# Optimization experiments

Measured on AMD Instinct MI355X. Metric: run time of the kernel, lower is better.

## Reference

```python
import jax, jax.numpy as jnp
import numpy as np

PI_2 = 3.14159 / 2  # matches the torch module's pi_2 constant
EPS = 1e-8          # F.cosine_similarity default eps


def setup_inputs() -> dict:
    key = jax.random.key(0)
    k1, k2 = jax.random.split(key)
    B, N, C, H, W = 32, 2000, 512, 7, 7
    key_t = jax.random.normal(k1, (B, C, H, W), dtype=jnp.float32)
    memory = jax.random.normal(k2, (N, C, H, W), dtype=jnp.float32)
    return {"key": key_t, "memory": memory}


def reference(key, memory):
    # Memory.read(key): cosine-similarity addressing + tan warp + softmax, then weighted read.
    B = key.shape[0]
    N = memory.shape[0]
    k = key.reshape(B, -1)        # [B, D], D = C*H*W
    m = memory.reshape(N, -1)     # [N, D]
    # cosine similarity with torch's eps clamping on norms
    dots = jnp.einsum('bd,nd->bn', k, m)                                   # [B, N]
    k_norm = jnp.maximum(jnp.sqrt(jnp.sum(k * k, axis=-1, keepdims=True)), EPS)  # [B, 1]
    m_norm = jnp.maximum(jnp.sqrt(jnp.sum(m * m, axis=-1)), EPS)                 # [N]
    cos = dots / (k_norm * m_norm[None, :])                                 # [B, N]
    w = jax.nn.softmax(jnp.tan(cos * PI_2), axis=1)                         # [B, N]
    # weighted read: sum_n w[b,n] * memory[n,c,h,w] -> [B, C, H, W]
    out = jnp.einsum('bn,nchw->bchw', w, memory)
    return out
```

## Files before the change

kernel.cpp:

```cpp
#include <hip/hip_runtime.h>
#include <math.h>

#define D_ELEMS 25088
#define D4      6272
#define N_MEM   2000
#define B_KEYS  32
#define PI_2F   1.570795f
#define EPSF    1e-8f
#define NSLICE  8
#define KSLICE  3136
#define KSTEPS  98

using short8 = __attribute__((ext_vector_type(8))) short;
using short4v = __attribute__((ext_vector_type(4))) short;
using f32x4  = __attribute__((ext_vector_type(4))) float;


__device__ inline short f2bf(float x) {
    union { float f; unsigned u; } v; v.f = x;
    unsigned r = v.u + 0x7fffu + ((v.u >> 16) & 1u);
    return (short)(r >> 16);
}

__global__ __launch_bounds__(256) void k_prep(const float* __restrict__ key,
                                              short* __restrict__ keyb) {
    const int i = blockIdx.x * 256 + threadIdx.x;
    const float4 f = ((const float4*)key)[i];
    short4v s; s[0] = f2bf(f.x); s[1] = f2bf(f.y); s[2] = f2bf(f.z); s[3] = f2bf(f.w);
    ((short4v*)keyb)[i] = s;
}

__global__ __launch_bounds__(64) void k_dots_mfma(const short* __restrict__ keyb,
                                                  const float* __restrict__ mem,
                                                  float* __restrict__ dots_part,
                                                  float* __restrict__ mn2_part) {
    const int nt   = blockIdx.x / NSLICE;
    const int s    = blockIdx.x % NSLICE;
    const int n0   = nt * 16;
    const int lane = threadIdx.x;
    const int quad = lane >> 4;
    const int l16  = lane & 15;
    const int k0   = s * KSLICE + quad * 8;

    const short* a0p = keyb + (size_t)l16 * D_ELEMS + k0;
    const short* a1p = keyb + (size_t)(16 + l16) * D_ELEMS + k0;
    const float4* bp = (const float4*)(mem + (size_t)(n0 + l16) * D_ELEMS + k0);

    f32x4 acc0 = {0.f, 0.f, 0.f, 0.f};
    f32x4 acc1 = {0.f, 0.f, 0.f, 0.f};
    float msq = 0.f;

    short8 a0 = *(const short8*)a0p;
    short8 a1 = *(const short8*)a1p;
    float4 f0 = bp[0], f1 = bp[1];

    for (int t = 0; t < KSTEPS; ++t) {
        const short8 a0c = a0, a1c = a1;
        const float4 f0c = f0, f1c = f1;
        if (t + 1 < KSTEPS) {
            const int ko = (t + 1) * 8;
            a0 = *(const short8*)(a0p + (t + 1) * 32);
            a1 = *(const short8*)(a1p + (t + 1) * 32);
            f0 = bp[ko]; f1 = bp[ko + 1];
        }
        msq += f0c.x * f0c.x + f0c.y * f0c.y + f0c.z * f0c.z + f0c.w * f0c.w
             + f1c.x * f1c.x + f1c.y * f1c.y + f1c.z * f1c.z + f1c.w * f1c.w;
        short8 b;
        b[0] = f2bf(f0c.x); b[1] = f2bf(f0c.y); b[2] = f2bf(f0c.z); b[3] = f2bf(f0c.w);
        b[4] = f2bf(f1c.x); b[5] = f2bf(f1c.y); b[6] = f2bf(f1c.z); b[7] = f2bf(f1c.w);
        acc0 = __builtin_amdgcn_mfma_f32_16x16x32_bf16(a0c, b, acc0, 0, 0, 0);
        acc1 = __builtin_amdgcn_mfma_f32_16x16x32_bf16(a1c, b, acc1, 0, 0, 0);
    }

    float* dp = dots_part + (size_t)(s * N_MEM + n0 + l16) * B_KEYS;
#pragma unroll
    for (int r = 0; r < 4; ++r) {
        dp[quad * 4 + r]      = acc0[r];
        dp[16 + quad * 4 + r] = acc1[r];
    }

    msq += __shfl_xor(msq, 16, 64);
    msq += __shfl_xor(msq, 32, 64);
    if (lane < 16) mn2_part[s * N_MEM + n0 + lane] = msq;
}

__global__ __launch_bounds__(512) void k_softmax(const float* __restrict__ key,
                                                 const float* __restrict__ dots_part,
                                                 const float* __restrict__ mn2_part,
                                                 float* __restrict__ w) {
    const int b   = blockIdx.x;
    const int tid = threadIdx.x;
    __shared__ float sred[512];
    __shared__ float xbuf[N_MEM];

    const float4* K4 = (const float4*)(key + (size_t)b * D_ELEMS);
    float ks = 0.f;
    for (int i = tid; i < D4; i += 512) {
        float4 kf = K4[i];
        ks += kf.x * kf.x + kf.y * kf.y + kf.z * kf.z + kf.w * kf.w;
    }
    sred[tid] = ks;
    __syncthreads();
    for (int o = 256; o; o >>= 1) {
        if (tid < o) sred[tid] += sred[tid + o];
        __syncthreads();
    }
    const float knorm = fmaxf(sqrtf(sred[0]), EPSF);
    __syncthreads();

    float mx = -1e30f;
    for (int n = tid; n < N_MEM; n += 512) {
        float ds = 0.f, ms = 0.f;
#pragma unroll
        for (int s = 0; s < NSLICE; ++s) ds += dots_part[(size_t)(s * N_MEM + n) * B_KEYS + b];
#pragma unroll
        for (int s = 0; s < NSLICE; ++s) ms += mn2_part[s * N_MEM + n];
        float mn = fmaxf(sqrtf(ms), EPSF);
        float x  = __tanf((ds / (knorm * mn)) * PI_2F);
        xbuf[n] = x;
        mx = fmaxf(mx, x);
    }
    sred[tid] = mx;
    __syncthreads();
    for (int o = 256; o; o >>= 1) {
        if (tid < o) sred[tid] = fmaxf(sred[tid], sred[tid + o]);
        __syncthreads();
    }
    mx = sred[0];
    __syncthreads();

    float sm = 0.f;
    for (int n = tid; n < N_MEM; n += 512) sm += __expf(xbuf[n] - mx);
    sred[tid] = sm;
    __syncthreads();
    for (int o = 256; o; o >>= 1) {
        if (tid < o) sred[tid] += sred[tid + o];
        __syncthreads();
    }
    const float inv = 1.f / sred[0];
    __syncthreads();

    for (int n = tid; n < N_MEM; n += 512)
        w[n * B_KEYS + b] = __expf(xbuf[n] - mx) * inv;
}

__global__ __launch_bounds__(256) void k_read(const float* __restrict__ mem,
                                              const float* __restrict__ w,
                                              float* __restrict__ partial,
                                              int nPerS) {
    const int db   = blockIdx.x % 98;
    const int s    = blockIdx.x / 98;
    const int n0   = s * nPerS;
    const int bg   = threadIdx.x >> 6;
    const int lane = threadIdx.x & 63;
    const int d4   = db * 64 + lane;

    const float4* M4 = (const float4*)mem;
    const float4* W4 = (const float4*)w;
    __shared__ float4 wls4[250 * 8];

    float acc[8][4];
#pragma unroll
    for (int i = 0; i < 8; ++i)
#pragma unroll
        for (int j = 0; j < 4; ++j) acc[i][j] = 0.f;

    for (int c0 = 0; c0 < nPerS; c0 += 250) {
        const int cn = min(250, nPerS - c0);
        __syncthreads();
        for (int i = threadIdx.x; i < cn * 8; i += 256)
            wls4[i] = W4[(n0 + c0) * 8 + i];
        __syncthreads();

        float4 mv = M4[(size_t)(n0 + c0) * D4 + d4];
        float4 wa = wls4[bg * 2];
        float4 wb = wls4[bg * 2 + 1];
        for (int nn = 0; nn < cn; ++nn) {
            const float4 mc = mv, wac = wa, wbc = wb;
            const int nx = (nn + 1 < cn) ? nn + 1 : nn;
            mv = M4[(size_t)(n0 + c0 + nx) * D4 + d4];
            wa = wls4[nx * 8 + bg * 2];
            wb = wls4[nx * 8 + bg * 2 + 1];
            const float wv[8] = {wac.x, wac.y, wac.z, wac.w,
                                 wbc.x, wbc.y, wbc.z, wbc.w};
#pragma unroll
            for (int i = 0; i < 8; ++i) {
                acc[i][0] += wv[i] * mc.x;
                acc[i][1] += wv[i] * mc.y;
                acc[i][2] += wv[i] * mc.z;
                acc[i][3] += wv[i] * mc.w;
            }
        }
    }

    float4* P4 = (float4*)partial;
#pragma unroll
    for (int i = 0; i < 8; ++i)
        P4[(size_t)(s * B_KEYS + bg * 8 + i) * D4 + d4] =
            make_float4(acc[i][0], acc[i][1], acc[i][2], acc[i][3]);
}

__global__ __launch_bounds__(256) void k_finish(const float* __restrict__ partial,
                                                float* __restrict__ out, int ns) {
    const int i = blockIdx.x * 256 + threadIdx.x;
    const float4* P4 = (const float4*)partial;
    float4 sum = P4[i];
    for (int s = 1; s < ns; ++s) {
        const float4 p = P4[(size_t)s * (B_KEYS * D4) + i];
        sum.x += p.x; sum.y += p.y; sum.z += p.z; sum.w += p.w;
    }
    ((float4*)out)[i] = sum;
}

extern "C" void kernel_launch(void* const* d_in, const int* in_sizes, int n_in,
                              void* d_out, int out_size, void* d_ws, size_t ws_size,
                              hipStream_t stream) {
    (void)in_sizes; (void)n_in; (void)out_size;
    const float* key = (const float*)d_in[0];
    const float* mem = (const float*)d_in[1];
    float* out = (float*)d_out;
    float* ws  = (float*)d_ws;

    short* keyb      = (short*)ws;
    float* dots_part = ws + 401408;
    float* mn2_part  = ws + 913408;
    float* w         = ws + 929408;
    float* part      = ws + 993408;

    int ns = 8;
    while (ns > 1 && (size_t)(993408 + (size_t)ns * 802816) * 4 > ws_size) ns >>= 1;
    const int nPerS = N_MEM / ns;

    k_prep     <<<784, 256, 0, stream>>>(key, keyb);
    k_dots_mfma<<<125 * NSLICE, 64, 0, stream>>>(keyb, mem, dots_part, mn2_part);
    k_softmax  <<<B_KEYS, 512, 0, stream>>>(key, dots_part, mn2_part, w);
    k_read     <<<98 * ns, 256, 0, stream>>>(mem, w, part, nPerS);
    k_finish   <<<784, 256, 0, stream>>>(part, out, ns);
}
```

Measured before the change: 420.3 us.

## Double K-split in dots kernel, add parallel reduce, unroll read loop by two

The MFMA dot kernel now splits the reduction dimension into 16 slices instead of 8, so it launches more blocks on the memory-bound first pass. A new k_reduce kernel sums the partial dots and norms across all threads, replacing the per-thread strided reduction inside the 32-block softmax kernel. The weighted-read kernel unrolls its loop by two with two memory prefetches in flight, fixes the chunk size at 250, and adds an occupancy hint of 3 blocks per SM. The cost is twice the partial-buffer traffic and one extra kernel launch.

```diff
diff --git a/kernel.cpp b/kernel.cpp
--- a/kernel.cpp
+++ b/kernel.cpp
@@ -7,9 +7,9 @@
 #define B_KEYS  32
 #define PI_2F   1.570795f
 #define EPSF    1e-8f
-#define NSLICE  8
-#define KSLICE  3136
-#define KSTEPS  98
+#define NSLICE  16
+#define KSLICE  1568
+#define KSTEPS  49
 
 using short8 = __attribute__((ext_vector_type(8))) short;
 using short4v = __attribute__((ext_vector_type(4))) short;
@@ -58,10 +58,10 @@
         const short8 a0c = a0, a1c = a1;
         const float4 f0c = f0, f1c = f1;
         if (t + 1 < KSTEPS) {
-            const int ko = (t + 1) * 8;
             a0 = *(const short8*)(a0p + (t + 1) * 32);
             a1 = *(const short8*)(a1p + (t + 1) * 32);
-            f0 = bp[ko]; f1 = bp[ko + 1];
+            f0 = bp[(t + 1) * 8];
+            f1 = bp[(t + 1) * 8 + 1];
         }
         msq += f0c.x * f0c.x + f0c.y * f0c.y + f0c.z * f0c.z + f0c.w * f0c.w
              + f1c.x * f1c.x + f1c.y * f1c.y + f1c.z * f1c.z + f1c.w * f1c.w;
@@ -84,9 +84,26 @@
     if (lane < 16) mn2_part[s * N_MEM + n0 + lane] = msq;
 }
 
+__global__ __launch_bounds__(256) void k_reduce(const float* __restrict__ dots_part,
+                                                const float* __restrict__ mn2_part,
+                                                float* __restrict__ dots,
+                                                float* __restrict__ mn2) {
+    const int gid = blockIdx.x * 256 + threadIdx.x;
+    float ds = 0.f;
+#pragma unroll
+    for (int s = 0; s < NSLICE; ++s) ds += dots_part[s * (N_MEM * B_KEYS) + gid];
+    dots[gid] = ds;
+    if (gid < N_MEM) {
+        float ms = 0.f;
+#pragma unroll
+        for (int s = 0; s < NSLICE; ++s) ms += mn2_part[s * N_MEM + gid];
+        mn2[gid] = ms;
+    }
+}
+
 __global__ __launch_bounds__(512) void k_softmax(const float* __restrict__ key,
-                                                 const float* __restrict__ dots_part,
-                                                 const float* __restrict__ mn2_part,
+                                                 const float* __restrict__ dots,
+                                                 const float* __restrict__ mn2,
                                                  float* __restrict__ w) {
     const int b   = blockIdx.x;
     const int tid = threadIdx.x;
@@ -110,13 +127,8 @@
 
     float mx = -1e30f;
     for (int n = tid; n < N_MEM; n += 512) {
-        float ds = 0.f, ms = 0.f;
-#pragma unroll
-        for (int s = 0; s < NSLICE; ++s) ds += dots_part[(size_t)(s * N_MEM + n) * B_KEYS + b];
-#pragma unroll
-        for (int s = 0; s < NSLICE; ++s) ms += mn2_part[s * N_MEM + n];
-        float mn = fmaxf(sqrtf(ms), EPSF);
-        float x  = __tanf((ds / (knorm * mn)) * PI_2F);
+        float mn = fmaxf(sqrtf(mn2[n]), EPSF);
+        float x  = __tanf((dots[n * B_KEYS + b] / (knorm * mn)) * PI_2F);
         xbuf[n] = x;
         mx = fmaxf(mx, x);
     }
@@ -144,10 +156,10 @@
         w[n * B_KEYS + b] = __expf(xbuf[n] - mx) * inv;
 }
 
-__global__ __launch_bounds__(256) void k_read(const float* __restrict__ mem,
-                                              const float* __restrict__ w,
-                                              float* __restrict__ partial,
-                                              int nPerS) {
+__global__ __launch_bounds__(256, 3) void k_read(const float* __restrict__ mem,
+                                                 const float* __restrict__ w,
+                                                 float* __restrict__ partial,
+                                                 int nPerS) {
     const int db   = blockIdx.x % 98;
     const int s    = blockIdx.x / 98;
     const int n0   = s * nPerS;
@@ -166,29 +178,45 @@
         for (int j = 0; j < 4; ++j) acc[i][j] = 0.f;
 
     for (int c0 = 0; c0 < nPerS; c0 += 250) {
-        const int cn = min(250, nPerS - c0);
+        const int cn = 250;
         __syncthreads();
         for (int i = threadIdx.x; i < cn * 8; i += 256)
             wls4[i] = W4[(n0 + c0) * 8 + i];
         __syncthreads();
 
-        float4 mv = M4[(size_t)(n0 + c0) * D4 + d4];
-        float4 wa = wls4[bg * 2];
-        float4 wb = wls4[bg * 2 + 1];
-        for (int nn = 0; nn < cn; ++nn) {
-            const float4 mc = mv, wac = wa, wbc = wb;
-            const int nx = (nn + 1 < cn) ? nn + 1 : nn;
-            mv = M4[(size_t)(n0 + c0 + nx) * D4 + d4];
-            wa = wls4[nx * 8 + bg * 2];
-            wb = wls4[nx * 8 + bg * 2 + 1];
-            const float wv[8] = {wac.x, wac.y, wac.z, wac.w,
-                                 wbc.x, wbc.y, wbc.z, wbc.w};
-#pragma unroll
-            for (int i = 0; i < 8; ++i) {
-                acc[i][0] += wv[i] * mc.x;
-                acc[i][1] += wv[i] * mc.y;
-                acc[i][2] += wv[i] * mc.z;
-                acc[i][3] += wv[i] * mc.w;
+        const float4* mp = M4 + (size_t)(n0 + c0) * D4 + d4;
+        float4 mv0 = mp[0];
+        float4 mv1 = mp[(size_t)D4];
+        for (int nn = 0; nn < cn; nn += 2) {
+            const float4 mc0 = mv0;
+            const int i2 = (nn + 2 < cn) ? nn + 2 : cn - 2;
+            mv0 = mp[(size_t)i2 * D4];
+            {
+                const float4 wa = wls4[nn * 8 + bg * 2];
+                const float4 wb = wls4[nn * 8 + bg * 2 + 1];
+                const float wv[8] = {wa.x, wa.y, wa.z, wa.w, wb.x, wb.y, wb.z, wb.w};
+#pragma unroll
+                for (int i = 0; i < 8; ++i) {
+                    acc[i][0] += wv[i] * mc0.x;
+                    acc[i][1] += wv[i] * mc0.y;
+                    acc[i][2] += wv[i] * mc0.z;
+                    acc[i][3] += wv[i] * mc0.w;
+                }
+            }
+            const float4 mc1 = mv1;
+            const int i3 = (nn + 3 < cn) ? nn + 3 : cn - 1;
+            mv1 = mp[(size_t)i3 * D4];
+            {
+                const float4 wa = wls4[(nn + 1) * 8 + bg * 2];
+                const float4 wb = wls4[(nn + 1) * 8 + bg * 2 + 1];
+                const float wv[8] = {wa.x, wa.y, wa.z, wa.w, wb.x, wb.y, wb.z, wb.w};
+#pragma unroll
+                for (int i = 0; i < 8; ++i) {
+                    acc[i][0] += wv[i] * mc1.x;
+                    acc[i][1] += wv[i] * mc1.y;
+                    acc[i][2] += wv[i] * mc1.z;
+                    acc[i][3] += wv[i] * mc1.w;
+                }
             }
         }
     }
@@ -223,17 +251,20 @@
 
     short* keyb      = (short*)ws;
     float* dots_part = ws + 401408;
-    float* mn2_part  = ws + 913408;
-    float* w         = ws + 929408;
-    float* part      = ws + 993408;
+    float* mn2_part  = ws + 1425408;
+    float* dots      = ws + 1457408;
+    float* mn2       = ws + 1521408;
+    float* w         = ws + 1523456;
+    float* part      = ws + 1587456;
 
     int ns = 8;
-    while (ns > 1 && (size_t)(993408 + (size_t)ns * 802816) * 4 > ws_size) ns >>= 1;
+    while (ns > 1 && (size_t)(1587456 + (size_t)ns * 802816) * 4 > ws_size) ns >>= 1;
     const int nPerS = N_MEM / ns;
 
     k_prep     <<<784, 256, 0, stream>>>(key, keyb);
     k_dots_mfma<<<125 * NSLICE, 64, 0, stream>>>(keyb, mem, dots_part, mn2_part);
-    k_softmax  <<<B_KEYS, 512, 0, stream>>>(key, dots_part, mn2_part, w);
+    k_reduce   <<<250, 256, 0, stream>>>(dots_part, mn2_part, dots, mn2);
+    k_softmax  <<<B_KEYS, 512, 0, stream>>>(key, dots, mn2, w);
     k_read     <<<98 * ns, 256, 0, stream>>>(mem, w, part, nPerS);
     k_finish   <<<784, 256, 0, stream>>>(part, out, ns);
 }
```

Result: faster. 396.9 us (-5.6%).
